# Optimization experiments

Measured on AMD Instinct MI355X. Metric: run time of the kernel, lower is better.

Reference implementation:

```python
import jax, jax.numpy as jnp
import numpy as np

K = 32   # tokens_per_obs (hard-coded in module)
V = 512  # vocab_size

def setup_inputs() -> dict:
    key = jax.random.key(0)
    ks = jax.random.split(key, 10)
    s = 0.02  # small init scale for numerical sanity
    return {
        "x": jax.random.normal(ks[0], (4096, 512), jnp.float32),
        "enc_w1": jax.random.normal(ks[1], (512, 512), jnp.float32) * s,
        "enc_b1": jnp.zeros((512,), jnp.float32),
        "enc_w2": jax.random.normal(ks[2], (512, 16384), jnp.float32) * s,
        "enc_b2": jnp.zeros((16384,), jnp.float32),
        "codebook": jax.random.uniform(ks[3], (16384, 256), jnp.float32, -1.0 / V, 1.0 / V),
        "dec_w1": jax.random.normal(ks[4], (256, 512), jnp.float32) * s,
        "dec_b1": jnp.zeros((512,), jnp.float32),
        "dec_w2": jax.random.normal(ks[5], (512, 512), jnp.float32) * s,
        "dec_b2": jnp.zeros((512,), jnp.float32),
    }

def reference(x, enc_w1, enc_b1, enc_w2, enc_b2, codebook,
              dec_w1, dec_b1, dec_w2, dec_b2):
    b = x.shape[0]
    # encoder MLP -> logits z of shape (b, K*V)
    h = jax.nn.relu(x @ enc_w1 + enc_b1)
    z = h @ enc_w2 + enc_b2
    zl = z.reshape(b, K, V)                      # (b, K, V) per-block logits
    # categorical sample per token block
    tokens = jax.random.categorical(jax.random.key(1), zl, axis=-1)  # (b, K) int
    p = jax.nn.softmax(zl, axis=-1).reshape(b, K * V)
    oh = jax.nn.one_hot(tokens, V, dtype=p.dtype).reshape(b, K * V)
    # straight-through: forward value == one-hot, gradient flows through p
    st = p + jax.lax.stop_gradient(oh - p)
    z_q = st @ codebook                          # (b, embed_dim) = sum of K code rows
    # decoder MLP -> reconstruction
    rec = jax.nn.relu(z_q @ dec_w1 + dec_b1) @ dec_w2 + dec_b2
    return z, z_q, rec
```

## Files before the change

### kernel.cpp

```cpp
#include <hip/hip_runtime.h>
#include <hip/hip_bf16.h>
#include <math.h>
#include <stdint.h>


#define BATCH 4096
#define KTOK  32
#define VOCAB 512
#define DMODEL 512
#define ZDIM  16384
#define EDIM  256
#define MARGIN 0.03125f

typedef __attribute__((ext_vector_type(8))) short short8v;
typedef __attribute__((ext_vector_type(4))) float f32x4;

__device__ __forceinline__ void threefry2x32(uint32_t k0, uint32_t k1,
                                             uint32_t x0, uint32_t x1,
                                             uint32_t& y0, uint32_t& y1) {
    uint32_t ks0 = k0, ks1 = k1, ks2 = k0 ^ k1 ^ 0x1BD11BDAu;
    x0 += ks0; x1 += ks1;
#define TFR(r) { x0 += x1; x1 = __builtin_rotateleft32(x1, r); x1 ^= x0; }
    TFR(13) TFR(15) TFR(26) TFR(6)
    x0 += ks1; x1 += ks2 + 1u;
    TFR(17) TFR(29) TFR(16) TFR(24)
    x0 += ks2; x1 += ks0 + 2u;
    TFR(13) TFR(15) TFR(26) TFR(6)
    x0 += ks0; x1 += ks1 + 3u;
    TFR(17) TFR(29) TFR(16) TFR(24)
    x0 += ks1; x1 += ks2 + 4u;
    TFR(13) TFR(15) TFR(26) TFR(6)
    x0 += ks2; x1 += ks0 + 5u;
#undef TFR
    y0 = x0; y1 = x1;
}

__device__ __forceinline__ void threefry4x(uint32_t e,
                                           uint32_t& o0, uint32_t& o1,
                                           uint32_t& o2, uint32_t& o3) {
    const uint32_t KS2 = 0x1BD11BDBu;
    uint32_t xa = 0u, ya = e + 1u;
    uint32_t xb = 0u, yb = e + 2u;
    uint32_t xc = 0u, yc = e + 3u;
    uint32_t xd = 0u, yd = e + 4u;
#define RR(r) \
    xa += ya; xb += yb; xc += yc; xd += yd; \
    ya = __builtin_rotateleft32(ya, r) ^ xa; \
    yb = __builtin_rotateleft32(yb, r) ^ xb; \
    yc = __builtin_rotateleft32(yc, r) ^ xc; \
    yd = __builtin_rotateleft32(yd, r) ^ xd;
    RR(13) RR(15) RR(26) RR(6)
    xa += 1u; xb += 1u; xc += 1u; xd += 1u;
    ya += KS2 + 1u; yb += KS2 + 1u; yc += KS2 + 1u; yd += KS2 + 1u;
    RR(17) RR(29) RR(16) RR(24)
    xa += KS2; xb += KS2; xc += KS2; xd += KS2;
    ya += 2u; yb += 2u; yc += 2u; yd += 2u;
    RR(13) RR(15) RR(26) RR(6)
    ya += 4u; yb += 4u; yc += 4u; yd += 4u;
    RR(17) RR(29) RR(16) RR(24)
    xa += 1u; xb += 1u; xc += 1u; xd += 1u;
    ya += KS2 + 4u; yb += KS2 + 4u; yc += KS2 + 4u; yd += KS2 + 4u;
    RR(13) RR(15) RR(26) RR(6)
    xa += KS2; xb += KS2; xc += KS2; xd += KS2;
    ya += 5u; yb += 5u; yc += 5u; yd += 5u;
#undef RR
    o0 = xa ^ ya; o1 = xb ^ yb; o2 = xc ^ yc; o3 = xd ^ yd;
}

__device__ __forceinline__ float jax_gumbel(uint64_t e) {
    const float TINY = 1.17549435e-38f;
    uint32_t y0, y1;
    threefry2x32(0u, 1u, (uint32_t)(e >> 32), (uint32_t)(e & 0xffffffffull), y0, y1);
    uint32_t bits = y0 ^ y1;
    float u = __uint_as_float(0x3f800000u | (bits >> 9)) - 1.0f;
    u = u * 1.0f + TINY;
    u = fmaxf(TINY, u);
    return -logf(-logf(u));
}

__device__ __forceinline__ float gumbel_from_bits(uint32_t bits) {
    const float TINY = 1.17549435e-38f;
    const float LN2 = 0.69314718056f;
    float f = __uint_as_float(0x3f800000u | (bits >> 9));
    float u = f - 1.0f;
    float d = 2.0f - f;
    u = fmaxf(u, TINY);
    float e_hw = -LN2 * __builtin_amdgcn_logf(u);
    float e_poly = d * fmaf(d, fmaf(d, 0.33333333f, 0.5f), 1.0f);
    float e = (d < 0.002f) ? e_poly : e_hw;
    return -LN2 * __builtin_amdgcn_logf(e);
}

__device__ __forceinline__ float fast_gumbel(uint32_t e32) {
    uint32_t y0, y1;
    threefry2x32(0u, 1u, 0u, e32, y0, y1);
    return gumbel_from_bits(y0 ^ y1);
}

__device__ __forceinline__ unsigned short f32_to_bf16_rne(float f) {
    uint32_t u = __float_as_uint(f);
    uint32_t r = (u + 0x7fffu + ((u >> 16) & 1u)) >> 16;
    return (unsigned short)r;
}

__device__ __forceinline__ void gload16(const unsigned short* src,
                                        unsigned short* lds_base) {
    __builtin_amdgcn_global_load_lds(
        (const __attribute__((address_space(1))) unsigned int*)src,
        (__attribute__((address_space(3))) unsigned int*)lds_base, 16, 0, 0);
}

template<bool RELU>
__global__ __launch_bounds__(256)
void gemm_f32_64(const float* __restrict__ A, const float* __restrict__ B,
                 const float* __restrict__ bias, float* __restrict__ C,
                 unsigned short* __restrict__ Cb,
                 int M, int N, int K) {
    constexpr int BK = 16;
    __shared__ __align__(16) float As[BK][68];
    __shared__ __align__(16) float Bs[BK][68];

    const int tid = threadIdx.x;
    const int tx = tid % 16;
    const int ty = tid / 16;
    const int brow = blockIdx.y * 64;
    const int bcol = blockIdx.x * 64;

    float acc[4][4] = {};

    for (int k0 = 0; k0 < K; k0 += BK) {
        {
            int r = tid >> 2, c4 = tid & 3;
            float4 v = *(const float4*)&A[(size_t)(brow + r) * K + k0 + c4 * 4];
            As[c4 * 4 + 0][r] = v.x;
            As[c4 * 4 + 1][r] = v.y;
            As[c4 * 4 + 2][r] = v.z;
            As[c4 * 4 + 3][r] = v.w;
        }
        {
            int r = tid >> 4, c4 = tid & 15;
            *(float4*)&Bs[r][c4 * 4] = *(const float4*)&B[(size_t)(k0 + r) * N + bcol + c4 * 4];
        }
        __syncthreads();

#pragma unroll
        for (int kk = 0; kk < BK; ++kk) {
            float a[4], b[4];
            *(float4*)&a[0] = *(const float4*)&As[kk][ty * 4];
            *(float4*)&b[0] = *(const float4*)&Bs[kk][tx * 4];
#pragma unroll
            for (int i = 0; i < 4; ++i)
#pragma unroll
                for (int j = 0; j < 4; ++j)
                    acc[i][j] = fmaf(a[i], b[j], acc[i][j]);
        }
        __syncthreads();
    }

#pragma unroll
    for (int i = 0; i < 4; ++i) {
        int row = brow + ty * 4 + i;
        int col = bcol + tx * 4;
        float4 v;
        v.x = acc[i][0] + bias[col + 0];
        v.y = acc[i][1] + bias[col + 1];
        v.z = acc[i][2] + bias[col + 2];
        v.w = acc[i][3] + bias[col + 3];
        if (RELU) {
            v.x = fmaxf(v.x, 0.0f); v.y = fmaxf(v.y, 0.0f);
            v.z = fmaxf(v.z, 0.0f); v.w = fmaxf(v.w, 0.0f);
        }
        *(float4*)&C[(size_t)row * N + col] = v;
        if (Cb) {
            ushort4 o;
            o.x = f32_to_bf16_rne(v.x);
            o.y = f32_to_bf16_rne(v.y);
            o.z = f32_to_bf16_rne(v.z);
            o.w = f32_to_bf16_rne(v.w);
            *(ushort4*)&Cb[(size_t)row * N + col] = o;
        }
    }
}

template<bool RELU>
__global__ __launch_bounds__(256)
void gemm_f32(const float* __restrict__ A, const float* __restrict__ B,
              const float* __restrict__ bias, float* __restrict__ C,
              int M, int N, int K) {
    constexpr int BM = 128, BN = 128, BK = 16, TM = 8, TN = 8;
    __shared__ __align__(16) float As[BK][BM + 4];
    __shared__ __align__(16) float Bs[BK][BN + 4];

    const int tid = threadIdx.x;
    const int tx = tid % (BN / TN);
    const int ty = tid / (BN / TN);
    const int brow = blockIdx.y * BM;
    const int bcol = blockIdx.x * BN;

    float acc[TM][TN] = {};

    for (int k0 = 0; k0 < K; k0 += BK) {
#pragma unroll
        for (int f = tid; f < BM * BK / 4; f += 256) {
            int r = f / (BK / 4);
            int c4 = f % (BK / 4);
            float4 v = *(const float4*)&A[(size_t)(brow + r) * K + k0 + c4 * 4];
            As[c4 * 4 + 0][r] = v.x;
            As[c4 * 4 + 1][r] = v.y;
            As[c4 * 4 + 2][r] = v.z;
            As[c4 * 4 + 3][r] = v.w;
        }
#pragma unroll
        for (int f = tid; f < BK * BN / 4; f += 256) {
            int r = f / (BN / 4);
            int c4 = f % (BN / 4);
            *(float4*)&Bs[r][c4 * 4] = *(const float4*)&B[(size_t)(k0 + r) * N + bcol + c4 * 4];
        }
        __syncthreads();

#pragma unroll
        for (int kk = 0; kk < BK; ++kk) {
            float a[TM], b[TN];
            *(float4*)&a[0] = *(const float4*)&As[kk][ty * TM];
            *(float4*)&a[4] = *(const float4*)&As[kk][ty * TM + 4];
            *(float4*)&b[0] = *(const float4*)&Bs[kk][tx * TN];
            *(float4*)&b[4] = *(const float4*)&Bs[kk][tx * TN + 4];
#pragma unroll
            for (int i = 0; i < TM; ++i)
#pragma unroll
                for (int j = 0; j < TN; ++j)
                    acc[i][j] = fmaf(a[i], b[j], acc[i][j]);
        }
        __syncthreads();
    }

#pragma unroll
    for (int i = 0; i < TM; ++i) {
        int row = brow + ty * TM + i;
#pragma unroll
        for (int j = 0; j < TN; j += 4) {
            int col = bcol + tx * TN + j;
            float4 v;
            v.x = acc[i][j + 0] + bias[col + 0];
            v.y = acc[i][j + 1] + bias[col + 1];
            v.z = acc[i][j + 2] + bias[col + 2];
            v.w = acc[i][j + 3] + bias[col + 3];
            if (RELU) {
                v.x = fmaxf(v.x, 0.0f); v.y = fmaxf(v.y, 0.0f);
                v.z = fmaxf(v.z, 0.0f); v.w = fmaxf(v.w, 0.0f);
            }
            *(float4*)&C[(size_t)row * N + col] = v;
        }
    }
}

__global__ __launch_bounds__(256)
void transpose_w2(const float* __restrict__ src, unsigned short* __restrict__ dstb,
                  float* __restrict__ dstf, int R, int C, int writeF) {
    __shared__ float tile[32][33];
    const int c0 = blockIdx.x * 32, r0 = blockIdx.y * 32;
    const int tx = threadIdx.x % 32, ty = threadIdx.x / 32;
#pragma unroll
    for (int i = ty; i < 32; i += 8)
        tile[i][tx] = src[(size_t)(r0 + i) * C + c0 + tx];
    __syncthreads();
#pragma unroll
    for (int i = ty; i < 32; i += 8) {
        float v = tile[tx][i];
        size_t o = (size_t)(c0 + i) * R + r0 + tx;
        dstb[o] = f32_to_bf16_rne(v);
        if (writeF) dstf[o] = v;
    }
}

template<bool RELU, bool WF32, bool WBF16>
__global__ __launch_bounds__(256)
void gemm_mfma(const unsigned short* __restrict__ A,
               const unsigned short* __restrict__ Bt,
               const float* __restrict__ bias,
               float* __restrict__ C, unsigned short* __restrict__ Cb,
               int M, int N, int K) {
    constexpr int BM = 128, BN = 128, BK = 32;
    constexpr int TSZ = BM * BK;
    __shared__ unsigned short As[3 * TSZ];
    __shared__ unsigned short Bs[3 * TSZ];

    const int lid = blockIdx.y * gridDim.x + blockIdx.x;
    const int xcd = lid & 7;
    const int kk2 = lid >> 3;
    const int rpx = gridDim.y >> 3;
    const int by = xcd * rpx + (kk2 % rpx);
    const int bx = kk2 / rpx;

    const int tid = threadIdx.x;
    const int wid = tid >> 6;
    const int lane = tid & 63;
    const int wr = wid >> 1, wc = wid & 1;
    const int l15 = lane & 15, lq = lane >> 4;
    const int brow = by * BM;
    const int bcol = bx * BN;

    const int g1 = tid;
    const int g2 = tid + 256;
    const size_t a1 = (size_t)(brow + (g1 >> 2)) * K + (g1 & 3) * 8;
    const size_t a2 = (size_t)(brow + (g2 >> 2)) * K + (g2 & 3) * 8;
    const size_t b1 = (size_t)(bcol + (g1 >> 2)) * K + (g1 & 3) * 8;
    const size_t b2 = (size_t)(bcol + (g2 >> 2)) * K + (g2 & 3) * 8;
    const int off1 = wid * 64 * 8;
    const int off2 = (256 + wid * 64) * 8;

    f32x4 acc[4][4];
#pragma unroll
    for (int m = 0; m < 4; ++m)
#pragma unroll
        for (int n = 0; n < 4; ++n) acc[m][n] = (f32x4){0.f, 0.f, 0.f, 0.f};

    const int NK = K / BK;

#define STAGE(kt, bufi) { \
    const int k0_ = (kt) * BK; \
    const int o_ = (bufi) * TSZ; \
    gload16(A + a1 + k0_, As + o_ + off1); \
    gload16(A + a2 + k0_, As + o_ + off2); \
    gload16(Bt + b1 + k0_, Bs + o_ + off1); \
    gload16(Bt + b2 + k0_, Bs + o_ + off2); }

    STAGE(0, 0)
    if (NK > 1) STAGE(1, 1)

    int buf = 0;
    for (int kt = 0; kt < NK; ++kt) {
        if (kt + 2 < NK) {
            int nb = buf + 2; if (nb >= 3) nb -= 3;
            STAGE(kt + 2, nb)
        }
        if (kt + 2 < NK)      asm volatile("s_waitcnt vmcnt(8)" ::: "memory");
        else if (kt + 1 < NK) asm volatile("s_waitcnt vmcnt(4)" ::: "memory");
        else                  asm volatile("s_waitcnt vmcnt(0)" ::: "memory");
        __builtin_amdgcn_s_barrier();
        __builtin_amdgcn_sched_barrier(0);

        const int cb = buf * TSZ;
        short8v af[4], bf[4];
#pragma unroll
        for (int m = 0; m < 4; ++m)
            af[m] = *(const short8v*)&As[cb + (wr * 64 + m * 16 + l15) * BK + lq * 8];
#pragma unroll
        for (int n = 0; n < 4; ++n)
            bf[n] = *(const short8v*)&Bs[cb + (wc * 64 + n * 16 + l15) * BK + lq * 8];
#pragma unroll
        for (int m = 0; m < 4; ++m)
#pragma unroll
            for (int n = 0; n < 4; ++n)
                acc[m][n] = __builtin_amdgcn_mfma_f32_16x16x32_bf16(
                    af[m], bf[n], acc[m][n], 0, 0, 0);
        __builtin_amdgcn_s_barrier();
        ++buf; if (buf == 3) buf = 0;
    }
#undef STAGE

#pragma unroll
    for (int m = 0; m < 4; ++m) {
#pragma unroll
        for (int n = 0; n < 4; ++n) {
            int col = bcol + wc * 64 + n * 16 + l15;
            float bv = bias[col];
#pragma unroll
            for (int r = 0; r < 4; ++r) {
                int row = brow + wr * 64 + m * 16 + lq * 4 + r;
                float v = acc[m][n][r] + bv;
                if (RELU) v = fmaxf(v, 0.0f);
                if (WF32) C[(size_t)row * N + col] = v;
                if (WBF16) Cb[(size_t)row * N + col] = f32_to_bf16_rne(v);
            }
        }
    }
}

__global__ __launch_bounds__(256)
void sample_tokens_max(const float* __restrict__ z, int* __restrict__ tokens,
                       float* __restrict__ s1v, int* __restrict__ amb,
                       int* __restrict__ ambCount) {
    const int wave = threadIdx.x >> 6;
    const int lane = threadIdx.x & 63;
    const uint32_t t = blockIdx.x * 4 + wave;
    const float* zr = z + (size_t)t * VOCAB;

    float sc[8];
    float m = -INFINITY;
#pragma unroll
    for (int half = 0; half < 2; ++half) {
        const int e0 = half * 256 + lane * 4;
        const float4 zv = *(const float4*)&zr[e0];
        uint32_t b0, b1, b2, b3;
        threefry4x(t * (uint32_t)VOCAB + (uint32_t)e0, b0, b1, b2, b3);
        sc[half * 4 + 0] = zv.x + gumbel_from_bits(b0);
        sc[half * 4 + 1] = zv.y + gumbel_from_bits(b1);
        sc[half * 4 + 2] = zv.z + gumbel_from_bits(b2);
        sc[half * 4 + 3] = zv.w + gumbel_from_bits(b3);
        m = fmaxf(m, fmaxf(fmaxf(sc[half * 4 + 0], sc[half * 4 + 1]),
                           fmaxf(sc[half * 4 + 2], sc[half * 4 + 3])));
    }
#pragma unroll
    for (int off = 32; off > 0; off >>= 1)
        m = fmaxf(m, __shfl_xor(m, off));

    const float thr = m - MARGIN;
    int nge = 0;
    int vsel = VOCAB;
#pragma unroll
    for (int idx = 0; idx < 8; ++idx) {
        unsigned long long mge = __ballot(sc[idx] >= thr);
        nge += __popcll(mge);
        unsigned long long meq = __ballot(sc[idx] == m);
        if (vsel == VOCAB && meq) {
            int ln = __builtin_ctzll(meq);
            vsel = (idx >> 2) * 256 + ln * 4 + (idx & 3);
        }
    }
    if (lane == 0) {
        tokens[t] = vsel;
        s1v[t] = m;
        if (nge >= 2) {
            int idx = atomicAdd(ambCount, 1);
            amb[idx] = (int)t;
        }
    }
}

__global__ __launch_bounds__(64)
void refine_tokens2(const float* __restrict__ z, const float* __restrict__ h,
                    const float* __restrict__ w2t, const float* __restrict__ eb2,
                    const int* __restrict__ amb, const int* __restrict__ ambCount,
                    const float* __restrict__ s1v, int* __restrict__ tok) {
    __shared__ float hrow[DMODEL];
    __shared__ int candv[64];
    const int cnt = *ambCount;
    const int lane = threadIdx.x;

    for (int i = blockIdx.x; i < cnt; i += gridDim.x) {
        const int t = amb[i];
        const int b = t >> 5;
        const int kb = t & 31;
        const float* zr = z + (size_t)t * VOCAB;
        const float s1 = s1v[t];

        {
            float4 hv0 = *(const float4*)&h[(size_t)b * DMODEL + lane * 8];
            float4 hv1 = *(const float4*)&h[(size_t)b * DMODEL + lane * 8 + 4];
            *(float4*)&hrow[lane * 8] = hv0;
            *(float4*)&hrow[lane * 8 + 4] = hv1;
        }

        int base = 0;
#pragma unroll
        for (int half = 0; half < 2; ++half) {
            int e0 = half * 256 + lane * 4;
            float4 zv = *(const float4*)&zr[e0];
            float zs[4] = {zv.x, zv.y, zv.z, zv.w};
#pragma unroll
            for (int j = 0; j < 4; ++j) {
                int v = e0 + j;
                float s = zs[j] + fast_gumbel((uint32_t)t * VOCAB + v);
                bool pred = (s >= s1 - MARGIN);
                unsigned long long mask = __ballot(pred);
                if (pred) {
                    int slot = base + __popcll(mask & ((1ull << lane) - 1ull));
                    if (slot < 64) candv[slot] = v;
                }
                base += __popcll(mask);
            }
        }
        __syncthreads();
        const int ncand = base < 64 ? base : 64;

        float bestE = -INFINITY;
        int bestV = VOCAB;
        if (lane < ncand) {
            const int v = candv[lane];
            const int n = kb * VOCAB + v;
            const float* wr_ = w2t + (size_t)n * DMODEL;
            float acc = 0.f;
#pragma unroll 8
            for (int k = 0; k < DMODEL; ++k)
                acc = fmaf(hrow[k], wr_[k], acc);
            bestE = acc + eb2[n] + jax_gumbel((uint64_t)t * VOCAB + v);
            bestV = v;
        }
#pragma unroll
        for (int off = 32; off > 0; off >>= 1) {
            float oe = __shfl_down(bestE, off);
            int ov = __shfl_down(bestV, off);
            if (oe > bestE || (oe == bestE && ov < bestV)) { bestE = oe; bestV = ov; }
        }
        if (lane == 0) tok[t] = bestV;
        __syncthreads();
    }
}

__global__ __launch_bounds__(256)
void sample_tokens_simple(const float* __restrict__ z, int* __restrict__ tokens) {
    const int wave = threadIdx.x >> 6;
    const int lane = threadIdx.x & 63;
    const size_t t = (size_t)blockIdx.x * 4 + wave;
    const float* zr = z + t * VOCAB;
    float zv[8];
    *(float4*)&zv[0] = *(const float4*)&zr[lane * 8];
    *(float4*)&zv[4] = *(const float4*)&zr[lane * 8 + 4];
    const uint64_t ebase = t * (uint64_t)VOCAB + (uint64_t)lane * 8;
    float best = -INFINITY;
    int bestv = 0;
#pragma unroll
    for (int j = 0; j < 8; ++j) {
        float g = jax_gumbel(ebase + j);
        float s = zv[j] + g;
        int v = lane * 8 + j;
        if (s > best || (s == best && v < bestv)) { best = s; bestv = v; }
    }
#pragma unroll
    for (int off = 32; off > 0; off >>= 1) {
        float ob = __shfl_down(best, off);
        int ov = __shfl_down(bestv, off);
        if (ob > best || (ob == best && ov < bestv)) { best = ob; bestv = ov; }
    }
    if (lane == 0) tokens[t] = bestv;
}

__global__ __launch_bounds__(64)
void zero_count(int* p) { if (threadIdx.x == 0) *p = 0; }

__global__ __launch_bounds__(256)
void gather_zq(const int* __restrict__ tokens, const float* __restrict__ codebook,
               float* __restrict__ zq, unsigned short* __restrict__ zqb) {
    const int b = blockIdx.x;
    const int d = threadIdx.x;
    float s = 0.0f;
#pragma unroll
    for (int k = 0; k < KTOK; ++k) {
        int tok = tokens[b * KTOK + k];
        s += codebook[(size_t)(k * VOCAB + tok) * EDIM + d];
    }
    zq[(size_t)b * EDIM + d] = s;
    if (zqb) zqb[(size_t)b * EDIM + d] = f32_to_bf16_rne(s);
}

extern "C" void kernel_launch(void* const* d_in, const int* in_sizes, int n_in,
                              void* d_out, int out_size, void* d_ws, size_t ws_size,
                              hipStream_t stream) {
    const float* x   = (const float*)d_in[0];
    const float* ew1 = (const float*)d_in[1];
    const float* eb1 = (const float*)d_in[2];
    const float* ew2 = (const float*)d_in[3];
    const float* eb2 = (const float*)d_in[4];
    const float* cb  = (const float*)d_in[5];
    const float* dw1 = (const float*)d_in[6];
    const float* db1 = (const float*)d_in[7];
    const float* dw2 = (const float*)d_in[8];
    const float* db2 = (const float*)d_in[9];

    float* out = (float*)d_out;
    float* z   = out;
    float* zq  = out + (size_t)BATCH * ZDIM;
    float* rec = zq + (size_t)BATCH * EDIM;

    char* ws = (char*)d_ws;
    float* h    = (float*)(ws);
    unsigned short* zqb   = (unsigned short*)(ws + 8388608);
    unsigned short* h2b   = (unsigned short*)(ws + 10485760);
    unsigned short* dw1tb = (unsigned short*)(ws + 14680064);
    unsigned short* dw2tb = (unsigned short*)(ws + 14942208);
    float* h2f  = (float*)(ws + 8388608);
    unsigned short* hb   = (unsigned short*)(ws + 16777216);
    unsigned short* w2bt = (unsigned short*)(ws + 20971520);
    float* w2t  = (float*)(ws + 37748736);
    char* tail = ws + 71303168;
    const size_t WS_NEED2 = 71303168 + 1572864 + 256;
    const bool fast2 = ws_size >= WS_NEED2;
    if (!fast2) tail = ws + 16777216;
    int*   tok  = (int*)(tail);
    float* s1v  = (float*)(tail + 524288);
    int*   amb  = (int*)(tail + 1048576);
    int*   cnt  = (int*)(tail + 1572864);

    dim3 blk(256);

    gemm_f32_64<true ><<<dim3(DMODEL / 64, BATCH / 64), blk, 0, stream>>>(
        x, ew1, eb1, h, fast2 ? hb : (unsigned short*)nullptr,
        BATCH, DMODEL, DMODEL);

    if (fast2) {
        transpose_w2<<<dim3(ZDIM / 32, DMODEL / 32), blk, 0, stream>>>(
            ew2, w2bt, w2t, DMODEL, ZDIM, 1);
        transpose_w2<<<dim3(DMODEL / 32, EDIM / 32), blk, 0, stream>>>(
            dw1, dw1tb, nullptr, EDIM, DMODEL, 0);
        transpose_w2<<<dim3(DMODEL / 32, DMODEL / 32), blk, 0, stream>>>(
            dw2, dw2tb, nullptr, DMODEL, DMODEL, 0);
        zero_count<<<dim3(1), dim3(64), 0, stream>>>(cnt);
        gemm_mfma<false, true, false><<<dim3(ZDIM / 128, BATCH / 128), blk, 0, stream>>>(
            hb, w2bt, eb2, z, nullptr, BATCH, ZDIM, DMODEL);
        sample_tokens_max<<<dim3(BATCH * KTOK / 4), blk, 0, stream>>>(
            z, tok, s1v, amb, cnt);
        refine_tokens2<<<dim3(4096), dim3(64), 0, stream>>>(
            z, h, w2t, eb2, amb, cnt, s1v, tok);
        gather_zq<<<dim3(BATCH), blk, 0, stream>>>(tok, cb, zq, zqb);
        gemm_mfma<true, false, true><<<dim3(DMODEL / 128, BATCH / 128), blk, 0, stream>>>(
            zqb, dw1tb, db1, nullptr, h2b, BATCH, DMODEL, EDIM);
        gemm_mfma<false, true, false><<<dim3(DMODEL / 128, BATCH / 128), blk, 0, stream>>>(
            h2b, dw2tb, db2, rec, nullptr, BATCH, DMODEL, DMODEL);
    } else {
        gemm_f32<false><<<dim3(ZDIM / 128, BATCH / 128), blk, 0, stream>>>(
            h, ew2, eb2, z, BATCH, ZDIM, DMODEL);
        sample_tokens_simple<<<dim3(BATCH * KTOK / 4), blk, 0, stream>>>(z, tok);
        gather_zq<<<dim3(BATCH), blk, 0, stream>>>(tok, cb, zq, nullptr);
        gemm_f32_64<true ><<<dim3(DMODEL / 64, BATCH / 64), blk, 0, stream>>>(
            zq, dw1, db1, h2f, nullptr, BATCH, DMODEL, EDIM);
        gemm_f32_64<false><<<dim3(DMODEL / 64, BATCH / 64), blk, 0, stream>>>(
            h2f, dw2, db2, rec, nullptr, BATCH, DMODEL, DMODEL);
    }
}
```

Before: 395.2 us.

## Fuse logits GEMM with Gumbel top-2 sampling in epilogue

The z-logits bf16 MFMA GEMM is merged with the Gumbel-max sampling pass. Each block walks the four 128-column sub-tiles of one 512-wide vocab group, adds Gumbel noise in registers, and keeps a running top-2 through shuffles and LDS, so a separate kernel no longer has to re-read the 256MB z tensor. The grid is remapped so blocks are spread across XCDs, and ambiguous tokens are now flagged by the top-2 gap rather than a count above a threshold. Costs are extra epilogue work (threefry, shuffles, syncs) inside the GEMM, and z stores use a strided per-lane pattern that may coalesce worse.

```diff
diff --git a/kernel.cpp b/kernel.cpp
--- a/kernel.cpp
+++ b/kernel.cpp
@@ -35,14 +35,15 @@
     y0 = x0; y1 = x1;
 }
 
-__device__ __forceinline__ void threefry4x(uint32_t e,
+__device__ __forceinline__ void threefry4w(uint32_t c0, uint32_t c1,
+                                           uint32_t c2, uint32_t c3,
                                            uint32_t& o0, uint32_t& o1,
                                            uint32_t& o2, uint32_t& o3) {
     const uint32_t KS2 = 0x1BD11BDBu;
-    uint32_t xa = 0u, ya = e + 1u;
-    uint32_t xb = 0u, yb = e + 2u;
-    uint32_t xc = 0u, yc = e + 3u;
-    uint32_t xd = 0u, yd = e + 4u;
+    uint32_t xa = 0u, ya = c0 + 1u;
+    uint32_t xb = 0u, yb = c1 + 1u;
+    uint32_t xc = 0u, yc = c2 + 1u;
+    uint32_t xd = 0u, yd = c3 + 1u;
 #define RR(r) \
     xa += ya; xb += yb; xc += yc; xd += yd; \
     ya = __builtin_rotateleft32(ya, r) ^ xa; \
@@ -103,6 +104,21 @@
     return (unsigned short)r;
 }
 
+__device__ __forceinline__ void top2_push(float& s1, float& s2, int& v1,
+                                          float s, int v) {
+    if (s > s1 || (s == s1 && v < v1)) { s2 = s1; s1 = s; v1 = v; }
+    else s2 = fmaxf(s2, s);
+}
+__device__ __forceinline__ void top2_merge(float& s1, float& s2, int& v1,
+                                           float os1, float os2, int ov1) {
+    if (os1 > s1 || (os1 == s1 && ov1 < v1)) {
+        s2 = fmaxf(s1, os2);
+        s1 = os1; v1 = ov1;
+    } else {
+        s2 = fmaxf(s2, os1);
+    }
+}
+
 __device__ __forceinline__ void gload16(const unsigned short* src,
                                         unsigned short* lds_base) {
     __builtin_amdgcn_global_load_lds(
@@ -377,53 +393,145 @@
     }
 }
 
-__global__ __launch_bounds__(256)
-void sample_tokens_max(const float* __restrict__ z, int* __restrict__ tokens,
-                       float* __restrict__ s1v, int* __restrict__ amb,
-                       int* __restrict__ ambCount) {
-    const int wave = threadIdx.x >> 6;
-    const int lane = threadIdx.x & 63;
-    const uint32_t t = blockIdx.x * 4 + wave;
-    const float* zr = z + (size_t)t * VOCAB;
-
-    float sc[8];
-    float m = -INFINITY;
-#pragma unroll
-    for (int half = 0; half < 2; ++half) {
-        const int e0 = half * 256 + lane * 4;
-        const float4 zv = *(const float4*)&zr[e0];
-        uint32_t b0, b1, b2, b3;
-        threefry4x(t * (uint32_t)VOCAB + (uint32_t)e0, b0, b1, b2, b3);
-        sc[half * 4 + 0] = zv.x + gumbel_from_bits(b0);
-        sc[half * 4 + 1] = zv.y + gumbel_from_bits(b1);
-        sc[half * 4 + 2] = zv.z + gumbel_from_bits(b2);
-        sc[half * 4 + 3] = zv.w + gumbel_from_bits(b3);
-        m = fmaxf(m, fmaxf(fmaxf(sc[half * 4 + 0], sc[half * 4 + 1]),
-                           fmaxf(sc[half * 4 + 2], sc[half * 4 + 3])));
-    }
-#pragma unroll
-    for (int off = 32; off > 0; off >>= 1)
-        m = fmaxf(m, __shfl_xor(m, off));
-
-    const float thr = m - MARGIN;
-    int nge = 0;
-    int vsel = VOCAB;
-#pragma unroll
-    for (int idx = 0; idx < 8; ++idx) {
-        unsigned long long mge = __ballot(sc[idx] >= thr);
-        nge += __popcll(mge);
-        unsigned long long meq = __ballot(sc[idx] == m);
-        if (vsel == VOCAB && meq) {
-            int ln = __builtin_ctzll(meq);
-            vsel = (idx >> 2) * 256 + ln * 4 + (idx & 3);
-        }
-    }
-    if (lane == 0) {
-        tokens[t] = vsel;
-        s1v[t] = m;
-        if (nge >= 2) {
-            int idx = atomicAdd(ambCount, 1);
-            amb[idx] = (int)t;
+__global__ __launch_bounds__(256, 4)
+void gemm_fused_topk(const unsigned short* __restrict__ A,
+                     const unsigned short* __restrict__ Bt,
+                     const float* __restrict__ bias,
+                     float* __restrict__ z,
+                     int* __restrict__ tokens, float* __restrict__ s1v,
+                     int* __restrict__ amb, int* __restrict__ ambCount,
+                     int K) {
+    constexpr int BM = 128, BK = 32, TSZ = BM * BK;
+    __shared__ unsigned short As[2 * TSZ];
+    __shared__ unsigned short Bs[2 * TSZ];
+    __shared__ float pS1[BM][2], pS2[BM][2];
+    __shared__ int   pV[BM][2];
+
+    const int lid = blockIdx.x;
+    const int xcd = lid & 7;
+    const int q = lid >> 3;
+    const int p = xcd * 4 + (q & 3);
+    const int grp = q >> 2;
+    const int brow = p * BM;
+
+    const int tid = threadIdx.x;
+    const int wid = tid >> 6;
+    const int lane = tid & 63;
+    const int wr = wid >> 1, wc = wid & 1;
+    const int l15 = lane & 15, lq = lane >> 4;
+
+    const int g1 = tid;
+    const int g2 = tid + 256;
+    const size_t a1 = (size_t)(brow + (g1 >> 2)) * K + (g1 & 3) * 8;
+    const size_t a2 = (size_t)(brow + (g2 >> 2)) * K + (g2 & 3) * 8;
+    const int off1 = wid * 64 * 8;
+    const int off2 = (256 + wid * 64) * 8;
+    const int NK = K / BK;
+
+    float rs1 = -INFINITY, rs2 = -INFINITY;
+    int rv1 = VOCAB;
+
+#pragma unroll 1
+    for (int sub = 0; sub < 4; ++sub) {
+        const int bcol = grp * 512 + sub * 128;
+        const size_t b1 = (size_t)(bcol + (g1 >> 2)) * K + (g1 & 3) * 8;
+        const size_t b2 = (size_t)(bcol + (g2 >> 2)) * K + (g2 & 3) * 8;
+
+        f32x4 acc[4][4];
+#pragma unroll
+        for (int m = 0; m < 4; ++m)
+#pragma unroll
+            for (int n = 0; n < 4; ++n) acc[m][n] = (f32x4){0.f, 0.f, 0.f, 0.f};
+
+#define STAGE(kt, bufi) { \
+    const int k0_ = (kt) * BK; \
+    const int o_ = (bufi) * TSZ; \
+    gload16(A + a1 + k0_, As + o_ + off1); \
+    gload16(A + a2 + k0_, As + o_ + off2); \
+    gload16(Bt + b1 + k0_, Bs + o_ + off1); \
+    gload16(Bt + b2 + k0_, Bs + o_ + off2); }
+
+        STAGE(0, 0)
+        __syncthreads();
+        int buf = 0;
+        for (int kt = 0; kt < NK; ++kt) {
+            if (kt + 1 < NK) STAGE(kt + 1, buf ^ 1)
+
+            const int cb = buf * TSZ;
+            short8v af[4], bf[4];
+#pragma unroll
+            for (int m = 0; m < 4; ++m)
+                af[m] = *(const short8v*)&As[cb + (wr * 64 + m * 16 + l15) * BK + lq * 8];
+#pragma unroll
+            for (int n = 0; n < 4; ++n)
+                bf[n] = *(const short8v*)&Bs[cb + (wc * 64 + n * 16 + l15) * BK + lq * 8];
+#pragma unroll
+            for (int m = 0; m < 4; ++m)
+#pragma unroll
+                for (int n = 0; n < 4; ++n)
+                    acc[m][n] = __builtin_amdgcn_mfma_f32_16x16x32_bf16(
+                        af[m], bf[n], acc[m][n], 0, 0, 0);
+            __syncthreads();
+            buf ^= 1;
+        }
+#undef STAGE
+
+        float bv[4];
+#pragma unroll
+        for (int n = 0; n < 4; ++n)
+            bv[n] = bias[bcol + wc * 64 + n * 16 + l15];
+
+#pragma unroll
+        for (int m = 0; m < 4; ++m) {
+#pragma unroll
+            for (int r = 0; r < 4; ++r) {
+                const int lrow = wr * 64 + m * 16 + lq * 4 + r;
+                const int row = brow + lrow;
+                const uint32_t t = (uint32_t)row * KTOK + grp;
+                const int vbase = sub * 128 + wc * 64 + l15;
+                float val[4];
+#pragma unroll
+                for (int n = 0; n < 4; ++n) {
+                    val[n] = acc[m][n][r] + bv[n];
+                    z[(size_t)row * ZDIM + (size_t)grp * VOCAB + vbase + n * 16] = val[n];
+                }
+                const uint32_t eb = t * (uint32_t)VOCAB + (uint32_t)vbase;
+                uint32_t b0, b1_, b2_, b3_;
+                threefry4w(eb, eb + 16, eb + 32, eb + 48, b0, b1_, b2_, b3_);
+                float s1 = -INFINITY, s2 = -INFINITY;
+                int v1 = VOCAB;
+                top2_push(s1, s2, v1, val[0] + gumbel_from_bits(b0),  vbase);
+                top2_push(s1, s2, v1, val[1] + gumbel_from_bits(b1_), vbase + 16);
+                top2_push(s1, s2, v1, val[2] + gumbel_from_bits(b2_), vbase + 32);
+                top2_push(s1, s2, v1, val[3] + gumbel_from_bits(b3_), vbase + 48);
+#pragma unroll
+                for (int off = 1; off < 16; off <<= 1) {
+                    float os1 = __shfl_xor(s1, off);
+                    float os2 = __shfl_xor(s2, off);
+                    int   ov1 = __shfl_xor(v1, off);
+                    top2_merge(s1, s2, v1, os1, os2, ov1);
+                }
+                if (l15 == 0) {
+                    pS1[lrow][wc] = s1; pS2[lrow][wc] = s2; pV[lrow][wc] = v1;
+                }
+            }
+        }
+        __syncthreads();
+        if (tid < BM) {
+            top2_merge(rs1, rs2, rv1, pS1[tid][0], pS2[tid][0], pV[tid][0]);
+            top2_merge(rs1, rs2, rv1, pS1[tid][1], pS2[tid][1], pV[tid][1]);
+        }
+        __syncthreads();
+    }
+
+    if (tid < BM) {
+        const int row = brow + tid;
+        const uint32_t t = (uint32_t)row * KTOK + grp;
+        tokens[t] = rv1;
+        s1v[t] = rs1;
+        if (rs1 - rs2 < MARGIN) {
+            int i = atomicAdd(ambCount, 1);
+            amb[i] = (int)t;
         }
     }
 }
@@ -596,10 +704,8 @@
         transpose_w2<<<dim3(DMODEL / 32, DMODEL / 32), blk, 0, stream>>>(
             dw2, dw2tb, nullptr, DMODEL, DMODEL, 0);
         zero_count<<<dim3(1), dim3(64), 0, stream>>>(cnt);
-        gemm_mfma<false, true, false><<<dim3(ZDIM / 128, BATCH / 128), blk, 0, stream>>>(
-            hb, w2bt, eb2, z, nullptr, BATCH, ZDIM, DMODEL);
-        sample_tokens_max<<<dim3(BATCH * KTOK / 4), blk, 0, stream>>>(
-            z, tok, s1v, amb, cnt);
+        gemm_fused_topk<<<dim3(1024), blk, 0, stream>>>(
+            hb, w2bt, eb2, z, tok, s1v, amb, cnt, DMODEL);
         refine_tokens2<<<dim3(4096), dim3(64), 0, stream>>>(
             z, h, w2t, eb2, amb, cnt, s1v, tok);
         gather_zq<<<dim3(BATCH), blk, 0, stream>>>(tok, cb, zq, zqb);
```

Result: slower. 433.5 us (+9.7%).
